# Optimization experiments

Measured on AMD Instinct MI355X. Metric: run time of the kernel, lower is better.

The kernel has to match this reference:

```python
import jax, jax.numpy as jnp
import numpy as np
import math

B, S, D, H = 2, 2048, 1024, 16
DH = D // H  # 64


def setup_inputs() -> dict:
    key = jax.random.key(0)
    ks = jax.random.split(key, 12)
    def nrm(k, shape, scale=1.0):
        return (jax.random.normal(k, shape, dtype=jnp.float32) * scale)
    return {
        "x": nrm(ks[0], (B, S, D)),
        "memory": nrm(ks[1], (B, S, D)),
        "mask": jax.random.randint(ks[2], (B, S), 0, 2).astype(jnp.bool_),
        "wq": nrm(ks[3], (D, D), 1.0 / math.sqrt(D)),
        "bq": nrm(ks[4], (D,), 0.02),
        "wk": nrm(ks[5], (D, D), 1.0 / math.sqrt(D)),
        "bk": nrm(ks[6], (D,), 0.02),
        "wv": nrm(ks[7], (D, D), 1.0 / math.sqrt(D)),
        "bv": nrm(ks[8], (D,), 0.02),
        "wo": nrm(ks[9], (D, D), 1.0 / math.sqrt(D)),
        "bo": nrm(ks[10], (D,), 0.02),
    }


def reference(x, memory, mask, wq, bq, wk, bk, wv, bv, wo, bo):
    b, s, d = x.shape
    def split(t):  # [b, s, d] -> [b, h, s, dh]
        return t.reshape(b, -1, H, DH).transpose(0, 2, 1, 3)
    q = split(x @ wq + bq) * (1.0 / math.sqrt(DH))
    k = split(memory @ wk + bk)
    v = split(memory @ wv + bv)
    logit = jnp.einsum("bhqd,bhkd->bhqk", q, k)
    neg_inf = jnp.finfo(logit.dtype).min
    logit = jnp.where(mask[:, None, None, :], -jnp.inf, logit)
    weights = jax.nn.softmax(logit, axis=-1)
    out = jnp.einsum("bhqk,bhkd->bhqd", weights, v)
    out = out.transpose(0, 2, 1, 3).reshape(b, -1, d)  # combine heads
    return out @ wo + bo
```

## Files before the change

### kernel.cpp

```cpp
#include <hip/hip_runtime.h>
#include <hip/hip_bf16.h>

#define B_  2
#define S_  2048
#define D_  1024
#define H_  16
#define DH_ 64
#define M_  (B_*S_)
#define KSTR 2048

typedef unsigned short ushort_t;
typedef __attribute__((ext_vector_type(8)))  short bf16x8;
typedef __attribute__((ext_vector_type(4)))  float f32x4;
typedef __attribute__((ext_vector_type(16))) float f32x16;
typedef __attribute__((ext_vector_type(4)))  int   i32x4;

#define MFMA16x16(A,Bb,C) __builtin_amdgcn_mfma_f32_16x16x32_bf16(A,Bb,C,0,0,0)
#define MFMA32(A,Bb,C)    __builtin_amdgcn_mfma_f32_32x32x16_bf16(A,Bb,C,0,0,0)
#define QSCALE 0.18033688011112042f
#define E2(x) __builtin_amdgcn_exp2f(x)
#define WVAL 0.00390625f

__device__ __forceinline__ ushort_t f2bf(float f) {
    return __builtin_bit_cast(ushort_t, __float2bfloat16(f));
}
__device__ __forceinline__ unsigned pack2(float a, float b) {
    return (unsigned)f2bf(a) | ((unsigned)f2bf(b) << 16);
}

__device__ __forceinline__ void gll16(const void* g, void* l) {
    __builtin_amdgcn_global_load_lds(
        (const __attribute__((address_space(1))) unsigned int*)g,
        (__attribute__((address_space(3))) unsigned int*)l, 16, 0, 0);
}

#define SWZ(row, c8) ((((c8) ^ ((row) & 7))) * 8)

__device__ __forceinline__ void pl32swap(int& a, int& b) {
    asm("v_permlane32_swap_b32 %0, %1" : "+v"(a), "+v"(b));
}

__global__ __launch_bounds__(256) void prep_all(const float* __restrict__ x,
                                                const float* __restrict__ mem,
                                                const unsigned char* __restrict__ mask_raw,
                                                const float* __restrict__ wq,
                                                const float* __restrict__ wk,
                                                const float* __restrict__ wv,
                                                const float* __restrict__ wo,
                                                const float* __restrict__ bk,
                                                const float* __restrict__ bv,
                                                ushort_t* __restrict__ xb,
                                                ushort_t* __restrict__ mb,
                                                ushort_t* __restrict__ wqT,
                                                ushort_t* __restrict__ wkT,
                                                ushort_t* __restrict__ wvT,
                                                ushort_t* __restrict__ woT,
                                                float* __restrict__ vwf,
                                                ushort_t* __restrict__ vwb,
                                                float* __restrict__ biasKV) {
    __shared__ ushort_t T[64][65];
    __shared__ int isBool;
    const int bid = blockIdx.x;
    const int tid = threadIdx.x;

    if (bid < 4096) {
        const int i = (bid & 2047) * 256 + tid;
        const float* src = (bid < 2048) ? x : mem;
        ushort_t*    dst = (bid < 2048) ? xb : mb;
        float4 a = *(const float4*)(src + (size_t)i * 8);
        float4 b = *(const float4*)(src + (size_t)i * 8 + 4);
        bf16x8 t;
        t[0] = (short)f2bf(a.x); t[1] = (short)f2bf(a.y);
        t[2] = (short)f2bf(a.z); t[3] = (short)f2bf(a.w);
        t[4] = (short)f2bf(b.x); t[5] = (short)f2bf(b.y);
        t[6] = (short)f2bf(b.z); t[7] = (short)f2bf(b.w);
        *(bf16x8*)(dst + (size_t)i * 8) = t;
    } else if (bid < 5120) {
        const int tt = bid - 4096;
        const int z = tt >> 8, rem = tt & 255;
        const int bi = rem >> 4, bj = rem & 15;
        const float* W; ushort_t* Wt;
        switch (z) {
            case 0:  W = wq; Wt = wqT; break;
            case 1:  W = wk; Wt = wkT; break;
            case 2:  W = wv; Wt = wvT; break;
            default: W = wo; Wt = woT; break;
        }
        const int r = tid >> 2;
        const int c = tid & 3;
        const float* src = W + (size_t)(bi * 64 + r) * D_ + bj * 64 + c * 16;
        #pragma unroll
        for (int qq = 0; qq < 4; qq++) {
            float4 v = *(const float4*)(src + qq * 4);
            T[r][c * 16 + qq * 4 + 0] = f2bf(v.x);
            T[r][c * 16 + qq * 4 + 1] = f2bf(v.y);
            T[r][c * 16 + qq * 4 + 2] = f2bf(v.z);
            T[r][c * 16 + qq * 4 + 3] = f2bf(v.w);
        }
        __syncthreads();
        ushort_t tmp[16];
        #pragma unroll
        for (int qq = 0; qq < 16; qq++) tmp[qq] = T[c * 16 + qq][r];
        ushort_t* dst = Wt + (size_t)(bj * 64 + r) * D_ + bi * 64 + c * 16;
        *(bf16x8*)(dst)     = *(bf16x8*)&tmp[0];
        *(bf16x8*)(dst + 8) = *(bf16x8*)&tmp[8];
    } else {
        if (tid == 0) isBool = 0;
        __syncthreads();
        int found = 0;
        for (int i = tid; i < M_; i += 256) {
            if ((i & 3) != 0 && mask_raw[i] != 0) found = 1;
        }
        if (found) atomicOr(&isBool, 1);
        __syncthreads();
        const int isb = isBool;
        for (int i = tid; i < M_; i += 256) {
            int m;
            if (isb) m = (mask_raw[i] != 0);
            else     m = (((const int*)mask_raw)[i] != 0);
            const float wv2 = m ? 0.0f : WVAL;
            vwf[i] = wv2;
            vwb[i] = f2bf(wv2);
        }
        for (int i = tid; i < D_; i += 256) {
            biasKV[i]      = bk[i];
            biasKV[D_ + i] = bv[i];
        }
    }
}

template<int MODE>
__device__ __forceinline__ void gemm_body(const ushort_t* __restrict__ A,
                                          const ushort_t* __restrict__ Bt,
                                          const float* __restrict__ bias,
                                          const float* __restrict__ vw,
                                          void* __restrict__ Cv,
                                          float scale, int N, int bm, int bn,
                                          ushort_t* lds) {
    ushort_t (*As)[64] = (ushort_t(*)[64])lds;
    ushort_t (*Bs)[64] = (ushort_t(*)[64])(lds + 8192);

    const int tid = threadIdx.x;
    const int l15 = tid & 15;
    const int g   = (tid & 63) >> 4;
    const int w   = tid >> 6;
    const int wr  = w >> 1;
    const int wc  = w & 1;

    f32x4 acc[4][4] = {};

    #pragma unroll 1
    for (int kt = 0; kt < D_; kt += 64) {
        __syncthreads();
        #pragma unroll
        for (int j = 0; j < 4; j++) {
            const int idx = tid + 256 * j;
            const int row = idx >> 3;
            const int c8  = idx & 7;
            gll16(A  + (size_t)(bm + row) * D_ + kt + c8 * 8,
                  (char*)&As[0][0] + idx * 16);
            gll16(Bt + (size_t)(bn + row) * D_ + kt + c8 * 8,
                  (char*)&Bs[0][0] + idx * 16);
        }
        __syncthreads();

        #pragma unroll
        for (int kk = 0; kk < 2; kk++) {
            bf16x8 a[4], b[4];
            #pragma unroll
            for (int m = 0; m < 4; m++)
                a[m] = *(bf16x8*)&As[wr * 64 + 16 * m + l15][kk * 32 + g * 8];
            #pragma unroll
            for (int n = 0; n < 4; n++)
                b[n] = *(bf16x8*)&Bs[wc * 64 + 16 * n + l15][kk * 32 + g * 8];
            #pragma unroll
            for (int m = 0; m < 4; m++)
                #pragma unroll
                for (int n = 0; n < 4; n++)
                    acc[m][n] = MFMA16x16(a[m], b[n], acc[m][n]);
        }
    }

    if (MODE != 2) {
        #pragma unroll
        for (int n = 0; n < 4; n++) {
            const int col = bn + wc * 64 + 16 * n + l15;
            const float bv = bias[col];
            #pragma unroll
            for (int m = 0; m < 4; m++) {
                #pragma unroll
                for (int r = 0; r < 4; r++) {
                    const int row = bm + wr * 64 + 16 * m + 4 * g + r;
                    const float val = (acc[m][n][r] + bv) * scale;
                    if (MODE == 1) ((ushort_t*)Cv)[(size_t)row * N + col] = f2bf(val);
                    else           ((float*)Cv)[(size_t)row * N + col] = val;
                }
            }
        }
    } else {
        __syncthreads();
        ushort_t (*T)[136] = (ushort_t(*)[136])lds;
        #pragma unroll
        for (int n = 0; n < 4; n++) {
            const int col_l = wc * 64 + 16 * n + l15;
            const float bv = bias[bn + col_l];
            #pragma unroll
            for (int m = 0; m < 4; m++) {
                #pragma unroll
                for (int r = 0; r < 4; r++) {
                    const int row_l = wr * 64 + 16 * m + 4 * g + r;
                    T[col_l][row_l] = f2bf((acc[m][n][r] + bv) * vw[bm + row_l]);
                }
            }
        }
        __syncthreads();
        const int tc = tid >> 1;
        const int rc = (tid & 1) * 64;
        const int col1 = bn + tc - 1024;
        const int hh = col1 >> 6, dh = col1 & 63;
        const int bb = bm >> 11;
        const int s0 = (bm & 2047) + rc;
        ushort_t* dst = (ushort_t*)Cv + ((size_t)(bb * H_ + hh) * DH_ + dh) * S_ + s0;
        #pragma unroll
        for (int c = 0; c < 8; c++)
            *(bf16x8*)(dst + c * 8) = *(const bf16x8*)&T[tc][rc + c * 8];
    }
}

__global__ __launch_bounds__(256) void gemm_qkv(const ushort_t* __restrict__ xb,
                                                const ushort_t* __restrict__ mb,
                                                const ushort_t* __restrict__ wqT,
                                                const ushort_t* __restrict__ wkvT,
                                                const float* __restrict__ bq,
                                                const float* __restrict__ biasKV,
                                                const float* __restrict__ vwf,
                                                ushort_t* __restrict__ qb,
                                                ushort_t* __restrict__ kg,
                                                ushort_t* __restrict__ vtg) {
    __shared__ ushort_t lds[17408];
    const int y  = blockIdx.y;
    const int bm = blockIdx.x * 128;
    if (y < 8)       gemm_body<1>(xb, wqT,  bq,     nullptr, qb,  QSCALE, D_, bm, y * 128, lds);
    else if (y < 16) gemm_body<1>(mb, wkvT, biasKV, nullptr, kg,  1.0f,   D_, bm, (y - 8) * 128, lds);
    else             gemm_body<2>(mb, wkvT, biasKV, vwf,     vtg, 1.0f,   KSTR, bm, 1024 + (y - 16) * 128, lds);
}

__global__ __launch_bounds__(256) void gemm_o(const ushort_t* __restrict__ ab,
                                              const ushort_t* __restrict__ woT,
                                              const float* __restrict__ bo,
                                              float* __restrict__ out) {
    __shared__ __attribute__((aligned(16))) ushort_t As[64][64];
    __shared__ __attribute__((aligned(16))) ushort_t Bs[128][64];

    const int tid = threadIdx.x;
    const int l15 = tid & 15;
    const int g   = (tid & 63) >> 4;
    const int w   = tid >> 6;
    const int wr  = w >> 1;
    const int wc  = w & 1;
    const int bm  = blockIdx.y * 64;
    const int bn  = blockIdx.x * 128;

    f32x4 acc[2][4] = {};

    #pragma unroll 1
    for (int kt = 0; kt < D_; kt += 64) {
        __syncthreads();
        #pragma unroll
        for (int j = 0; j < 2; j++) {
            const int idx = tid + 256 * j;
            const int row = idx >> 3;
            const int c8  = idx & 7;
            gll16(ab + (size_t)(bm + row) * D_ + kt + c8 * 8,
                  (char*)&As[0][0] + idx * 16);
        }
        #pragma unroll
        for (int j = 0; j < 4; j++) {
            const int idx = tid + 256 * j;
            const int row = idx >> 3;
            const int c8  = idx & 7;
            gll16(woT + (size_t)(bn + row) * D_ + kt + c8 * 8,
                  (char*)&Bs[0][0] + idx * 16);
        }
        __syncthreads();

        #pragma unroll
        for (int kk = 0; kk < 2; kk++) {
            bf16x8 a[2], b[4];
            #pragma unroll
            for (int m = 0; m < 2; m++)
                a[m] = *(bf16x8*)&As[wr * 32 + 16 * m + l15][kk * 32 + g * 8];
            #pragma unroll
            for (int n = 0; n < 4; n++)
                b[n] = *(bf16x8*)&Bs[wc * 64 + 16 * n + l15][kk * 32 + g * 8];
            #pragma unroll
            for (int m = 0; m < 2; m++)
                #pragma unroll
                for (int n = 0; n < 4; n++)
                    acc[m][n] = MFMA16x16(a[m], b[n], acc[m][n]);
        }
    }

    #pragma unroll
    for (int n = 0; n < 4; n++) {
        const int col = bn + wc * 64 + 16 * n + l15;
        const float bv = bo[col];
        #pragma unroll
        for (int m = 0; m < 2; m++) {
            #pragma unroll
            for (int r = 0; r < 4; r++) {
                const int row = bm + wr * 32 + 16 * m + 4 * g + r;
                out[(size_t)row * D_ + col] = acc[m][n][r] + bv;
            }
        }
    }
}

#define KB 128
#define NT (S_ / KB)

__global__ __launch_bounds__(256) void attn_mfma(const ushort_t* __restrict__ q,
                                                 const ushort_t* __restrict__ kg,
                                                 const ushort_t* __restrict__ vtg,
                                                 const ushort_t* __restrict__ vwb,
                                                 ushort_t* __restrict__ o) {
    __shared__ __attribute__((aligned(16))) ushort_t Ks[2][KB][64];
    __shared__ __attribute__((aligned(16))) ushort_t Vt[2][DH_][KB];

    const int tid = threadIdx.x;
    const int w   = tid >> 6;
    const int l31 = tid & 31;
    const int hi  = (tid >> 5) & 1;

    const int blk = blockIdx.x;
    const int qt  = blk >> 5;
    const int bh  = blk & 31;
    const int h   = bh & 15;
    const int b   = bh >> 4;

    const int qr0 = qt * 128 + w * 32;
    const size_t hoff  = (size_t)h * DH_;
    const size_t kbase = (size_t)(b * S_) * D_ + hoff;
    const size_t vbase = (size_t)((b * H_ + h) * DH_) * S_;

    const int krow0 = tid >> 3, kc8 = tid & 7;
    const int vrow0 = tid >> 4, vc8 = tid & 15;

    bf16x8 qf[4];
    {
        const ushort_t* qp = q + (size_t)(b * S_ + qr0 + l31) * D_ + hoff + hi * 8;
        #pragma unroll
        for (int ks = 0; ks < 4; ks++)
            qf[ks] = *(const bf16x8*)(qp + ks * 16);
    }

    f32x16 oacc0 = {}, oacc1 = {};
    f32x16 dacc  = {};

    const ushort_t* wrow = vwb + b * S_ + 8 * hi;

    bf16x8 kreg[4], vreg[4];

    #pragma unroll
    for (int j = 0; j < 4; j++) {
        kreg[j] = *(const bf16x8*)&kg[kbase + (size_t)(krow0 + 32 * j) * D_ + kc8 * 8];
        vreg[j] = *(const bf16x8*)&vtg[vbase + (size_t)(vrow0 + 16 * j) * S_ + vc8 * 8];
    }
    #pragma unroll
    for (int j = 0; j < 4; j++) {
        const int kr = krow0 + 32 * j;
        const int vr = vrow0 + 16 * j;
        *(bf16x8*)&Ks[0][kr][SWZ(kr, kc8)] = kreg[j];
        *(bf16x8*)&Vt[0][vr][SWZ(vr, vc8)] = vreg[j];
    }
    #pragma unroll
    for (int j = 0; j < 4; j++) {
        kreg[j] = *(const bf16x8*)&kg[kbase + (size_t)(KB + krow0 + 32 * j) * D_ + kc8 * 8];
        vreg[j] = *(const bf16x8*)&vtg[vbase + (size_t)(vrow0 + 16 * j) * S_ + KB + vc8 * 8];
    }

    int cur = 0;
    #pragma unroll 1
    for (int t = 0; t < NT; t++) {
        __syncthreads();

        if (t + 1 < NT) {
            const int nb = cur ^ 1;
            #pragma unroll
            for (int j = 0; j < 4; j++) {
                const int kr = krow0 + 32 * j;
                const int vr = vrow0 + 16 * j;
                *(bf16x8*)&Ks[nb][kr][SWZ(kr, kc8)] = kreg[j];
                *(bf16x8*)&Vt[nb][vr][SWZ(vr, vc8)] = vreg[j];
            }
        }
        if (t + 2 < NT) {
            const size_t nk = (size_t)(t + 2) * KB;
            #pragma unroll
            for (int j = 0; j < 4; j++) {
                kreg[j] = *(const bf16x8*)&kg[kbase + (nk + krow0 + 32 * j) * D_ + kc8 * 8];
                vreg[j] = *(const bf16x8*)&vtg[vbase + (size_t)(vrow0 + 16 * j) * S_ + nk + vc8 * 8];
            }
        }

        #pragma unroll
        for (int kb = 0; kb < 4; kb++) {
            f32x16 st = {};
            __builtin_amdgcn_s_setprio(1);
            #pragma unroll
            for (int ks = 0; ks < 4; ks++) {
                const int row = 32 * kb + l31;
                bf16x8 kf = *(bf16x8*)&Ks[cur][row][SWZ(row, 2 * ks + hi)];
                st = MFMA32(kf, qf[ks], st);
            }
            __builtin_amdgcn_s_setprio(0);

            float p[16];
            p[0]  = E2(st[0]);  p[1]  = E2(st[1]);
            p[2]  = E2(st[2]);  p[3]  = E2(st[3]);
            p[4]  = E2(st[4]);  p[5]  = E2(st[5]);
            p[6]  = E2(st[6]);  p[7]  = E2(st[7]);
            p[8]  = E2(st[8]);  p[9]  = E2(st[9]);
            p[10] = E2(st[10]); p[11] = E2(st[11]);
            p[12] = E2(st[12]); p[13] = E2(st[13]);
            p[14] = E2(st[14]); p[15] = E2(st[15]);

            int ax0 = (int)pack2(p[0],  p[1]),  ay0 = (int)pack2(p[2],  p[3]);
            int az0 = (int)pack2(p[4],  p[5]),  aw0 = (int)pack2(p[6],  p[7]);
            int ax1 = (int)pack2(p[8],  p[9]),  ay1 = (int)pack2(p[10], p[11]);
            int az1 = (int)pack2(p[12], p[13]), aw1 = (int)pack2(p[14], p[15]);
            pl32swap(ax0, az0);
            pl32swap(ay0, aw0);
            pl32swap(ax1, az1);
            pl32swap(ay1, aw1);
            i32x4 t0, t1;
            t0[0] = ax0; t0[1] = ay0; t0[2] = az0; t0[3] = aw0;
            t1[0] = ax1; t1[1] = ay1; t1[2] = az1; t1[3] = aw1;
            bf16x8 pa0 = __builtin_bit_cast(bf16x8, t0);
            bf16x8 pa1 = __builtin_bit_cast(bf16x8, t1);

            const int kwoff = t * KB + 32 * kb;
            bf16x8 wf0 = *(const bf16x8*)(wrow + kwoff);
            bf16x8 wf1 = *(const bf16x8*)(wrow + kwoff + 16);

            const int vr0 = l31, vr1 = 32 + l31;
            bf16x8 v00 = *(bf16x8*)&Vt[cur][vr0][SWZ(vr0, 4 * kb + hi)];
            bf16x8 v01 = *(bf16x8*)&Vt[cur][vr0][SWZ(vr0, 4 * kb + 2 + hi)];
            bf16x8 v10 = *(bf16x8*)&Vt[cur][vr1][SWZ(vr1, 4 * kb + hi)];
            bf16x8 v11 = *(bf16x8*)&Vt[cur][vr1][SWZ(vr1, 4 * kb + 2 + hi)];
            __builtin_amdgcn_s_setprio(1);
            oacc0 = MFMA32(pa0, v00, oacc0);
            oacc0 = MFMA32(pa1, v01, oacc0);
            oacc1 = MFMA32(pa0, v10, oacc1);
            oacc1 = MFMA32(pa1, v11, oacc1);
            dacc  = MFMA32(pa0, wf0, dacc);
            dacc  = MFMA32(pa1, wf1, dacc);
            __builtin_amdgcn_s_setprio(0);
        }

        cur ^= 1;
    }

    #pragma unroll
    for (int reg = 0; reg < 16; reg++) {
        const int qrow = (reg & 3) + 8 * (reg >> 2) + 4 * hi;
        const float ivr = 1.f / dacc[reg];
        ushort_t* op = o + (size_t)(b * S_ + qr0 + qrow) * D_ + hoff;
        op[l31]      = f2bf(oacc0[reg] * ivr);
        op[32 + l31] = f2bf(oacc1[reg] * ivr);
    }
}

extern "C" void kernel_launch(void* const* d_in, const int* in_sizes, int n_in,
                              void* d_out, int out_size, void* d_ws, size_t ws_size,
                              hipStream_t stream) {
    const float* x      = (const float*)d_in[0];
    const float* memory = (const float*)d_in[1];
    const unsigned char* mask = (const unsigned char*)d_in[2];
    const float* wq = (const float*)d_in[3];
    const float* bq = (const float*)d_in[4];
    const float* wk = (const float*)d_in[5];
    const float* bk = (const float*)d_in[6];
    const float* wv = (const float*)d_in[7];
    const float* bv = (const float*)d_in[8];
    const float* wo = (const float*)d_in[9];
    const float* bo = (const float*)d_in[10];
    float* out = (float*)d_out;

    const size_t CH = (size_t)M_ * D_;
    const size_t WH = (size_t)D_ * D_;
    ushort_t* ws   = (ushort_t*)d_ws;
    ushort_t* xb   = ws;
    ushort_t* mb   = xb + CH;
    ushort_t* qb   = mb + CH;
    ushort_t* kg   = qb + CH;
    ushort_t* vtg  = kg + CH;
    ushort_t* ab   = vtg + CH;
    ushort_t* wqT  = ab + CH;
    ushort_t* wkT  = wqT + WH;
    ushort_t* wvT  = wkT + WH;
    ushort_t* woT  = wvT + WH;
    float* vwf     = (float*)(woT + WH);
    float* biasKV  = vwf + M_;
    ushort_t* vwb  = (ushort_t*)(biasKV + KSTR);

    prep_all<<<5121, 256, 0, stream>>>(x, memory, mask, wq, wk, wv, wo, bk, bv,
                                       xb, mb, wqT, wkT, wvT, woT, vwf, vwb, biasKV);

    gemm_qkv<<<dim3(32, 24), 256, 0, stream>>>(xb, mb, wqT, wkT, bq, biasKV, vwf,
                                               qb, kg, vtg);

    attn_mfma<<<B_ * H_ * (S_ / 128), 256, 0, stream>>>(qb, kg, vtg, vwb, ab);

    gemm_o<<<dim3(8, 64), 256, 0, stream>>>(ab, woT, bo, out);
}
```

Before: 145.3 us.

## Use direct global-to-LDS loads in attention and remap QKV GEMM blocks per XCD

The attention kernel's K/V staging now uses direct global-to-LDS 16-byte loads (gll16) with an XOR swizzle computed at load time. This replaces the register-staged prefetch two tiles ahead followed by LDS stores, and moves the barrier to the end of each tile iteration. Separately, the QKV GEMM launches as a 1D grid and remaps block IDs so that consecutive blocks on each XCD share column tiles, aiming for better L2 reuse. The gain is lower VGPR pressure and fewer instructions, at the cost of a shallower prefetch distance. There is also a risk that the async loads are not properly waited on before the barrier.

Measured after the change: 151.9 us. 1.05x slower.

```diff
diff --git a/kernel.cpp b/kernel.cpp
--- a/kernel.cpp
+++ b/kernel.cpp
@@ -238,8 +238,10 @@
                                                 ushort_t* __restrict__ kg,
                                                 ushort_t* __restrict__ vtg) {
     __shared__ ushort_t lds[17408];
-    const int y  = blockIdx.y;
-    const int bm = blockIdx.x * 128;
+    const int orig = blockIdx.x;
+    const int wg = (orig & 7) * 96 + (orig >> 3);
+    const int y  = wg >> 5;
+    const int bm = (wg & 31) * 128;
     if (y < 8)       gemm_body<1>(xb, wqT,  bq,     nullptr, qb,  QSCALE, D_, bm, y * 128, lds);
     else if (y < 16) gemm_body<1>(mb, wkvT, biasKV, nullptr, kg,  1.0f,   D_, bm, (y - 8) * 128, lds);
     else             gemm_body<2>(mb, wkvT, biasKV, vwf,     vtg, 1.0f,   KSTR, bm, 1024 + (y - 16) * 128, lds);
@@ -319,6 +321,23 @@
 #define KB 128
 #define NT (S_ / KB)
 
+__device__ __forceinline__ void stage_tile(const ushort_t* __restrict__ kg,
+                                           const ushort_t* __restrict__ vtg,
+                                           size_t kbase, size_t vbase, int koff,
+                                           int tid, ushort_t* ksb, ushort_t* vtb) {
+    #pragma unroll
+    for (int j = 0; j < 4; j++) {
+        const int kr = 32 * j + (tid >> 3);
+        const int kc = (tid & 7) ^ (kr & 7);
+        gll16(kg + kbase + (size_t)(koff + kr) * D_ + kc * 8,
+              (char*)ksb + (256 * j + tid) * 16);
+        const int vr = 16 * j + (tid >> 4);
+        const int vc = (tid & 15) ^ (vr & 7);
+        gll16(vtg + vbase + (size_t)vr * S_ + koff + vc * 8,
+              (char*)vtb + (256 * j + tid) * 16);
+    }
+}
+
 __global__ __launch_bounds__(256) void attn_mfma(const ushort_t* __restrict__ q,
                                                  const ushort_t* __restrict__ kg,
                                                  const ushort_t* __restrict__ vtg,
@@ -343,9 +362,6 @@
     const size_t kbase = (size_t)(b * S_) * D_ + hoff;
     const size_t vbase = (size_t)((b * H_ + h) * DH_) * S_;
 
-    const int krow0 = tid >> 3, kc8 = tid & 7;
-    const int vrow0 = tid >> 4, vc8 = tid & 15;
-
     bf16x8 qf[4];
     {
         const ushort_t* qp = q + (size_t)(b * S_ + qr0 + l31) * D_ + hoff + hi * 8;
@@ -359,49 +375,15 @@
 
     const ushort_t* wrow = vwb + b * S_ + 8 * hi;
 
-    bf16x8 kreg[4], vreg[4];
-
-    #pragma unroll
-    for (int j = 0; j < 4; j++) {
-        kreg[j] = *(const bf16x8*)&kg[kbase + (size_t)(krow0 + 32 * j) * D_ + kc8 * 8];
-        vreg[j] = *(const bf16x8*)&vtg[vbase + (size_t)(vrow0 + 16 * j) * S_ + vc8 * 8];
-    }
-    #pragma unroll
-    for (int j = 0; j < 4; j++) {
-        const int kr = krow0 + 32 * j;
-        const int vr = vrow0 + 16 * j;
-        *(bf16x8*)&Ks[0][kr][SWZ(kr, kc8)] = kreg[j];
-        *(bf16x8*)&Vt[0][vr][SWZ(vr, vc8)] = vreg[j];
-    }
-    #pragma unroll
-    for (int j = 0; j < 4; j++) {
-        kreg[j] = *(const bf16x8*)&kg[kbase + (size_t)(KB + krow0 + 32 * j) * D_ + kc8 * 8];
-        vreg[j] = *(const bf16x8*)&vtg[vbase + (size_t)(vrow0 + 16 * j) * S_ + KB + vc8 * 8];
-    }
+    stage_tile(kg, vtg, kbase, vbase, 0, tid, &Ks[0][0][0], &Vt[0][0][0]);
+    __syncthreads();
 
     int cur = 0;
     #pragma unroll 1
     for (int t = 0; t < NT; t++) {
-        __syncthreads();
-
-        if (t + 1 < NT) {
-            const int nb = cur ^ 1;
-            #pragma unroll
-            for (int j = 0; j < 4; j++) {
-                const int kr = krow0 + 32 * j;
-                const int vr = vrow0 + 16 * j;
-                *(bf16x8*)&Ks[nb][kr][SWZ(kr, kc8)] = kreg[j];
-                *(bf16x8*)&Vt[nb][vr][SWZ(vr, vc8)] = vreg[j];
-            }
-        }
-        if (t + 2 < NT) {
-            const size_t nk = (size_t)(t + 2) * KB;
-            #pragma unroll
-            for (int j = 0; j < 4; j++) {
-                kreg[j] = *(const bf16x8*)&kg[kbase + (nk + krow0 + 32 * j) * D_ + kc8 * 8];
-                vreg[j] = *(const bf16x8*)&vtg[vbase + (size_t)(vrow0 + 16 * j) * S_ + nk + vc8 * 8];
-            }
-        }
+        if (t + 1 < NT)
+            stage_tile(kg, vtg, kbase, vbase, (t + 1) * KB, tid,
+                       &Ks[cur ^ 1][0][0], &Vt[cur ^ 1][0][0]);
 
         #pragma unroll
         for (int kb = 0; kb < 4; kb++) {
@@ -458,6 +440,7 @@
             __builtin_amdgcn_s_setprio(0);
         }
 
+        __syncthreads();
         cur ^= 1;
     }
 
@@ -507,8 +490,8 @@
     prep_all<<<5121, 256, 0, stream>>>(x, memory, mask, wq, wk, wv, wo, bk, bv,
                                        xb, mb, wqT, wkT, wvT, woT, vwf, vwb, biasKV);
 
-    gemm_qkv<<<dim3(32, 24), 256, 0, stream>>>(xb, mb, wqT, wkT, bq, biasKV, vwf,
-                                               qb, kg, vtg);
+    gemm_qkv<<<768, 256, 0, stream>>>(xb, mb, wqT, wkT, bq, biasKV, vwf,
+                                      qb, kg, vtg);
 
     attn_mfma<<<B_ * H_ * (S_ / 128), 256, 0, stream>>>(qb, kg, vtg, vwb, ab);
 
```
